# Kernel tuning notes

Measured on AMD Instinct MI355X. Metric: run time of the kernel, lower is better.

The kernel has to match this reference:

```python
import jax, jax.numpy as jnp
import numpy as np

SCALE = 2
K_UP = 5
K_ENC = 3


def _conv(x, w, b, pad):
    # NCHW conv, OIHW weights
    y = jax.lax.conv_general_dilated(
        x, w, window_strides=(1, 1), padding=((pad, pad), (pad, pad)),
        dimension_numbers=('NCHW', 'OIHW', 'NCHW'))
    return y + b[None, :, None, None]


def setup_inputs() -> dict:
    key = jax.random.key(0)
    k0, k1, k2 = jax.random.split(key, 3)
    b, c, h, w = 4, 256, 64, 64
    c_mid = 64
    n_kernel = SCALE * SCALE * K_UP * K_UP  # 100
    x = jax.random.normal(k0, (b, c, h, w), jnp.float32)
    w1 = jax.random.normal(k1, (c_mid, c, K_ENC, K_ENC), jnp.float32) * 0.02
    b1 = jnp.zeros((c_mid,), jnp.float32)
    w2 = jax.random.normal(k2, (n_kernel, c_mid, 1, 1), jnp.float32) * 0.02
    b2 = jnp.zeros((n_kernel,), jnp.float32)
    return {"x": x, "w1": w1, "b1": b1, "w2": w2, "b2": b2}


def reference(x, w1, b1, w2, b2):
    b, c, h, w = x.shape
    s, k = SCALE, K_UP
    # kernel prediction encoder: 3x3 conv -> ReLU -> 1x1 conv
    feat = jax.nn.relu(_conv(x, w1, b1, K_ENC // 2))
    kern = _conv(feat, w2, b2, 0)                     # (b, s^2*k^2, h, w)
    kern = jax.nn.softmax(kern, axis=1)               # softmax over full channel dim (as in source)
    kern = kern.reshape(b, s * s, k * k, h, w)
    # F.unfold(x, k, padding=k//2) -> (b, c, k^2, h, w); torch ordering: kh major, kw minor
    pad = k // 2
    xp = jnp.pad(x, ((0, 0), (0, 0), (pad, pad), (pad, pad)))
    patches = jnp.stack([xp[:, :, i:i + h, j:j + w]
                         for i in range(k) for j in range(k)], axis=2)  # (b, c, k^2, h, w)
    # per-pixel weighted reassembly: sum over k^2 neighborhood
    out = jnp.einsum('bskhw,bckhw->bschw', kern, patches)  # (b, s^2, c, h, w)
    # view(b, s^2*c, h, w) then pixel_shuffle(scale), exactly matching torch semantics
    out = out.reshape(b, s * s * c, h, w)
    cout = (s * s * c) // (s * s)
    out = out.reshape(b, cout, s, s, h, w)
    out = out.transpose(0, 1, 4, 2, 5, 3).reshape(b, cout, h * s, w * s)
    return out
```

## Files before the change

kernel.cpp:

```cpp
#include <hip/hip_runtime.h>


#define BB 4
#define CC 256
#define HH 64
#define WW 64
#define CMID 64
#define NKCH 100

typedef __bf16 bf16;
typedef __bf16 bf16x8 __attribute__((ext_vector_type(8)));
typedef float f32x4 __attribute__((ext_vector_type(4)));

__device__ __forceinline__ void async_copy16(const void* gsrc, void* ldst) {
    __builtin_amdgcn_global_load_lds(
        (__attribute__((address_space(1))) void*)(void*)gsrc,
        (__attribute__((address_space(3))) void*)ldst, 16, 0, 0);
}

__global__ void k0a_transform(const float* __restrict__ w1, bf16* __restrict__ w1c) {
    int c8 = blockIdx.x;
    int oq = blockIdx.y;
    int tid = threadIdx.x;
    __shared__ __align__(16) float wf[16 * 300];

    for (int i = tid; i < 16 * 72; i += 256) {
        int o = i / 72, r = i % 72;
        *(float4*)&wf[o * 300 + r * 4] =
            *(const float4*)&w1[(size_t)(oq * 16 + o) * 2304 + c8 * 288 + r * 4];
    }
    __syncthreads();

    for (int t = tid; t < 576; t += 256) {
        int o = t & 15, q = (t >> 4) & 3, kk = t >> 6;
        union { bf16 h[8]; uint4 u; } v;
        #pragma unroll
        for (int i8 = 0; i8 < 8; ++i8)
            v.h[i8] = (bf16)wf[o * 300 + (q * 8 + i8) * 9 + kk];
        *(uint4*)&w1c[(size_t)((((c8 * 9 + kk) * 4 + q) * 64) + oq * 16 + o) * 8] = v.u;
    }
}

__global__ __launch_bounds__(512) void k12_fused(const float* __restrict__ x,
        const bf16* __restrict__ w1c, const float* __restrict__ b1,
        const float* __restrict__ w2, const float* __restrict__ b2,
        float* __restrict__ kern) {
    int bh = blockIdx.x;
    int b = bh >> 6, h = bh & 63;
    int tid = threadIdx.x;
    int lane = tid & 63, wid = tid >> 6;
    int l15 = lane & 15, quad = lane >> 4;
    int mhalf = wid & 1, nq = wid >> 1;

    __shared__ __align__(16) char smem[99072];
    bf16*  xs   = (bf16*)smem;
    bf16*  wlds = (bf16*)(smem + 15872);
    float* kts  = (float*)(smem + 15872);
    float* fs   = (float*)(smem + 52736);
    float* ws2  = (float*)(smem + 69376);
    float* red  = (float*)(smem + 94976);

    for (int i = tid; i < 1600; i += 512)
        *(float4*)&ws2[i * 4] = *(const float4*)&w2[i * 4];

    for (int i = tid; i < 3 * 66 * 40; i += 512) xs[i] = (bf16)0.f;

    const float* xb = x + (size_t)b * (CC * HH * WW);

    int ppp[6], rrr[6];
    bool vmask[6];
    #pragma unroll
    for (int j = 0; j < 6; ++j) {
        int task = wid + j * 8;
        ppp[j] = task & 15;
        rrr[j] = task >> 4;
        int hr = h - 1 + rrr[j];
        vmask[j] = (hr >= 0 && hr < HH);
    }

    float f0[6], f1[6];
    #define LOADX(C8)                                                            \
        _Pragma("unroll")                                                        \
        for (int j = 0; j < 6; ++j) {                                            \
            if (vmask[j]) {                                                      \
                const float* src = xb + ((size_t)((C8) * 32 + 2 * ppp[j]) * (HH * WW)) \
                                 + (h - 1 + rrr[j]) * WW + lane;                 \
                f0[j] = src[0]; f1[j] = src[HH * WW];                            \
            }                                                                    \
        }

    LOADX(0)
    __syncthreads();

    f32x4 acc0 = {0.f, 0.f, 0.f, 0.f}, acc1 = {0.f, 0.f, 0.f, 0.f};

    for (int c8 = 0; c8 < 8; ++c8) {
        for (int t = wid; t < 36; t += 8)
            async_copy16(w1c + (((c8 * 36 + t) << 9) + lane * 8), (void*)&wlds[t << 9]);
        #pragma unroll
        for (int j = 0; j < 6; ++j) {
            if (vmask[j]) {
                union { bf16 hh[2]; unsigned u; } cv;
                cv.hh[0] = (bf16)f0[j]; cv.hh[1] = (bf16)f1[j];
                *(unsigned*)&xs[(rrr[j] * 66 + 1 + lane) * 40 + 2 * ppp[j]] = cv.u;
            }
        }
        __syncthreads();
        if (c8 < 7) { LOADX(c8 + 1) }
        #pragma unroll
        for (int kk = 0; kk < 9; ++kk) {
            int r3 = kk / 3, kw = kk % 3;
            bf16x8 a0 = *(const bf16x8*)&wlds[((kk * 4 + quad) * 64 + mhalf * 32 + l15) * 8];
            bf16x8 a1 = *(const bf16x8*)&wlds[((kk * 4 + quad) * 64 + mhalf * 32 + 16 + l15) * 8];
            bf16x8 xv = *(const bf16x8*)&xs[(r3 * 66 + nq * 16 + l15 + kw) * 40 + quad * 8];
            acc0 = __builtin_amdgcn_mfma_f32_16x16x32_bf16(a0, xv, acc0, 0, 0, 0);
            acc1 = __builtin_amdgcn_mfma_f32_16x16x32_bf16(a1, xv, acc1, 0, 0, 0);
        }
        __syncthreads();
    }

    int px = nq * 16 + l15;
    #pragma unroll
    for (int mi = 0; mi < 2; ++mi) {
        int oc0 = mhalf * 32 + mi * 16 + quad * 4;
        float4 bv = *(const float4*)&b1[oc0];
        f32x4 v = mi ? acc1 : acc0;
        fs[(oc0 + 0) * 65 + px] = fmaxf(v[0] + bv.x, 0.f);
        fs[(oc0 + 1) * 65 + px] = fmaxf(v[1] + bv.y, 0.f);
        fs[(oc0 + 2) * 65 + px] = fmaxf(v[2] + bv.z, 0.f);
        fs[(oc0 + 3) * 65 + px] = fmaxf(v[3] + bv.w, 0.f);
    }
    __syncthreads();

    int w = lane;
    int g = wid, s2 = g & 3, ihalf = g >> 2;
    int i0 = ihalf ? 13 : 0;

    float4 fv[16];
    #pragma unroll
    for (int q = 0; q < 16; ++q) {
        fv[q].x = fs[(4 * q + 0) * 65 + w];
        fv[q].y = fs[(4 * q + 1) * 65 + w];
        fv[q].z = fs[(4 * q + 2) * 65 + w];
        fv[q].w = fs[(4 * q + 3) * 65 + w];
    }

    float lg[13];
    #pragma unroll
    for (int ii = 0; ii < 13; ++ii) {
        int idx = i0 + ii;
        bool act = (idx < 25);
        int oc = s2 * 25 + (act ? idx : 0);
        float a = b2[oc];
        const float4* wr = (const float4*)&ws2[oc * 64];
        #pragma unroll
        for (int q = 0; q < 16; ++q) {
            float4 wv = wr[q];
            a += fv[q].x * wv.x + fv[q].y * wv.y + fv[q].z * wv.z + fv[q].w * wv.w;
        }
        lg[ii] = act ? a : -1e30f;
    }

    float m = -1e30f;
    #pragma unroll
    for (int ii = 0; ii < 13; ++ii) m = fmaxf(m, lg[ii]);
    red[g * 64 + w] = m;
    __syncthreads();
    m = fmaxf(fmaxf(fmaxf(red[0 * 64 + w], red[1 * 64 + w]),
                    fmaxf(red[2 * 64 + w], red[3 * 64 + w])),
              fmaxf(fmaxf(red[4 * 64 + w], red[5 * 64 + w]),
                    fmaxf(red[6 * 64 + w], red[7 * 64 + w])));
    float ssum = 0.f;
    #pragma unroll
    for (int ii = 0; ii < 13; ++ii) { lg[ii] = __expf(lg[ii] - m); ssum += lg[ii]; }
    red[512 + g * 64 + w] = ssum;
    __syncthreads();
    ssum = ((red[512 + 0 * 64 + w] + red[512 + 1 * 64 + w]) +
            (red[512 + 2 * 64 + w] + red[512 + 3 * 64 + w])) +
           ((red[512 + 4 * 64 + w] + red[512 + 5 * 64 + w]) +
            (red[512 + 6 * 64 + w] + red[512 + 7 * 64 + w]));
    float inv = 1.f / ssum;
    #pragma unroll
    for (int ii = 0; ii < 13; ++ii)
        if (i0 + ii < 25) kts[((i0 + ii) * 64 + w) * 4 + s2] = lg[ii] * inv;
    __syncthreads();

    float* kout = kern + (size_t)bh * 6400;
    for (int i = tid; i < 1600; i += 512)
        *(float4*)&kout[i * 4] = *(const float4*)&kts[i * 4];
    #undef LOADX
}

__global__ __launch_bounds__(256, 5) void k3_reassemble(const float* __restrict__ x,
        const float* __restrict__ kern, float* __restrict__ out) {
    int chunk = blockIdx.x;
    int bh = blockIdx.y;
    int b = bh >> 6, h = bh & 63;
    int tid = threadIdx.x;
    int w = tid & 63;
    int cg = tid >> 6;

    __shared__ __align__(16) float xs[5 * 68 * 20];

    for (int i = tid; i < 16 * 5 * 64; i += 256) {
        int ww = i & 63;
        int rr = (i >> 6) % 5;
        int cc = i / 320;
        int hr = h - 2 + rr;
        float v = (hr >= 0 && hr < HH)
            ? x[(((size_t)b * CC + chunk * 16 + cc) * HH + hr) * WW + ww] : 0.f;
        xs[(rr * 68 + 2 + ww) * 20 + cc] = v;
    }
    for (int i = tid; i < 320; i += 256) {
        int cc = i & 15;
        int q = (i >> 4) & 3;
        int rr = i >> 6;
        int slot = (q < 2) ? q : (q + 64);
        xs[(rr * 68 + slot) * 20 + cc] = 0.f;
    }

    const float* kp = kern + (size_t)bh * 6400 + w * 4;

    f32x4 kv0[5];
    #pragma unroll
    for (int kw = 0; kw < 5; ++kw)
        kv0[kw] = *(const f32x4*)&kp[kw * 256];

    __syncthreads();

    f32x4 a0 = {0.f,0.f,0.f,0.f}, a1 = {0.f,0.f,0.f,0.f};
    f32x4 a2 = {0.f,0.f,0.f,0.f}, a3 = {0.f,0.f,0.f,0.f};
    int cg4 = cg * 4;
    #pragma unroll
    for (int r = 0; r < 5; ++r) {
        #pragma unroll
        for (int kw = 0; kw < 5; ++kw) {
            f32x4 kv = (r == 0) ? kv0[kw]
                                : *(const f32x4*)&kp[(r * 5 + kw) * 256];
            f32x4 xv = *(const f32x4*)&xs[(r * 68 + w + kw) * 20 + cg4];
            a0 += kv.x * xv;
            a1 += kv.y * xv;
            a2 += kv.z * xv;
            a3 += kv.w * xv;
        }
    }

    int cq = chunk * 4 + cg;
    f32x4 accs[4] = {a0, a1, a2, a3};
    #pragma unroll
    for (int s = 0; s < 4; ++s) {
        size_t base = (((size_t)b * 256 + s * 64 + cq) * 128 + 2 * h) * 128 + 2 * w;
        *(float2*)&out[base]       = make_float2(accs[s][0], accs[s][1]);
        *(float2*)&out[base + 128] = make_float2(accs[s][2], accs[s][3]);
    }
}

extern "C" void kernel_launch(void* const* d_in, const int* in_sizes, int n_in,
                              void* d_out, int out_size, void* d_ws, size_t ws_size,
                              hipStream_t stream) {
    const float* x  = (const float*)d_in[0];
    const float* w1 = (const float*)d_in[1];
    const float* b1 = (const float*)d_in[2];
    const float* w2 = (const float*)d_in[3];
    const float* b2 = (const float*)d_in[4];
    float* out = (float*)d_out;

    char* wsb = (char*)d_ws;
    float* kern = (float*)wsb;
    bf16*  w1c  = (bf16*)(wsb + 6553600);

    k0a_transform<<<dim3(8, 4), 256, 0, stream>>>(w1, w1c);
    k12_fused<<<dim3(BB * HH), 512, 0, stream>>>(x, w1c, b1, w2, b2, kern);
    k3_reassemble<<<dim3(16, BB * HH), 256, 0, stream>>>(x, kern, out);
}
```

Measured before the change: 142.0 us.

## Double-buffer conv tiles, drop w2 LDS staging, swizzle reassembly LDS layout

The fused conv kernel now keeps two LDS buffers for both the x tile and the weight tile. The async weight copy and global x loads for the next channel chunk run while the MFMAs work on the current chunk, and each chunk pair needs fewer barriers. The w2 LDS staging is removed and the 1x1 conv reads w2 straight from global memory, which frees LDS for the second buffers. The reassembly kernel loads x as float4, stores it in a per-channel-group layout with an XOR swizzle to cut bank conflicts, and raises its occupancy hint from 5 to 6 blocks per CU. The larger LDS footprint may lower occupancy of the fused kernel.

```diff
diff --git a/kernel.cpp b/kernel.cpp
--- a/kernel.cpp
+++ b/kernel.cpp
@@ -52,18 +52,14 @@
     int l15 = lane & 15, quad = lane >> 4;
     int mhalf = wid & 1, nq = wid >> 1;
 
-    __shared__ __align__(16) char smem[99072];
-    bf16*  xs   = (bf16*)smem;
-    bf16*  wlds = (bf16*)(smem + 15872);
-    float* kts  = (float*)(smem + 15872);
-    float* fs   = (float*)(smem + 52736);
-    float* ws2  = (float*)(smem + 69376);
-    float* red  = (float*)(smem + 94976);
-
-    for (int i = tid; i < 1600; i += 512)
-        *(float4*)&ws2[i * 4] = *(const float4*)&w2[i * 4];
-
-    for (int i = tid; i < 3 * 66 * 40; i += 512) xs[i] = (bf16)0.f;
+    __shared__ __align__(16) char smem[122112];
+    bf16*  xs0  = (bf16*)smem;
+    bf16*  xs1  = (bf16*)(smem + 15872);
+    bf16*  wl0  = (bf16*)(smem + 31744);
+    bf16*  wl1  = (bf16*)(smem + 68608);
+    float* fs   = (float*)(smem + 105472);
+    float* kts  = (float*)(smem + 31744);
+    float* red  = (float*)smem;
 
     const float* xb = x + (size_t)b * (CC * HH * WW);
 
@@ -78,44 +74,59 @@
         vmask[j] = (hr >= 0 && hr < HH);
     }
 
-    float f0[6], f1[6];
-    #define LOADX(C8)                                                            \
+    float fA0[6], fA1[6], fB0[6], fB1[6];
+    #define LOADX(C8, F0, F1)                                                    \
         _Pragma("unroll")                                                        \
         for (int j = 0; j < 6; ++j) {                                            \
             if (vmask[j]) {                                                      \
                 const float* src = xb + ((size_t)((C8) * 32 + 2 * ppp[j]) * (HH * WW)) \
                                  + (h - 1 + rrr[j]) * WW + lane;                 \
-                f0[j] = src[0]; f1[j] = src[HH * WW];                            \
+                F0[j] = src[0]; F1[j] = src[HH * WW];                            \
             }                                                                    \
         }
-
-    LOADX(0)
+    #define WRITEB(F0, F1, XSDST)                                                \
+        _Pragma("unroll")                                                        \
+        for (int j = 0; j < 6; ++j) {                                            \
+            if (vmask[j]) {                                                      \
+                union { bf16 hh[2]; unsigned u; } cv;                            \
+                cv.hh[0] = (bf16)F0[j]; cv.hh[1] = (bf16)F1[j];                  \
+                *(unsigned*)&XSDST[(rrr[j] * 66 + 1 + lane) * 40 + 2 * ppp[j]] = cv.u; \
+            }                                                                    \
+        }
+    #define ACOPY(C8, WDST)                                                      \
+        for (int t = wid; t < 36; t += 8)                                        \
+            async_copy16(w1c + ((((C8) * 36 + t) << 9) + lane * 8), (void*)&WDST[t << 9]);
+    #define MFMAS(XSRC, WSRC)                                                    \
+        _Pragma("unroll")                                                        \
+        for (int kk = 0; kk < 9; ++kk) {                                         \
+            int r3 = kk / 3, kw = kk % 3;                                        \
+            bf16x8 a0 = *(const bf16x8*)&WSRC[((kk * 4 + quad) * 64 + mhalf * 32 + l15) * 8]; \
+            bf16x8 a1 = *(const bf16x8*)&WSRC[((kk * 4 + quad) * 64 + mhalf * 32 + 16 + l15) * 8]; \
+            bf16x8 xv = *(const bf16x8*)&XSRC[(r3 * 66 + nq * 16 + l15 + kw) * 40 + quad * 8]; \
+            acc0 = __builtin_amdgcn_mfma_f32_16x16x32_bf16(a0, xv, acc0, 0, 0, 0); \
+            acc1 = __builtin_amdgcn_mfma_f32_16x16x32_bf16(a1, xv, acc1, 0, 0, 0); \
+        }
+
+    for (int i = tid; i < 7936; i += 512) { xs0[i] = (bf16)0.f; xs1[i] = (bf16)0.f; }
+    LOADX(0, fA0, fA1)
+    ACOPY(0, wl0)
+    __syncthreads();
+    WRITEB(fA0, fA1, xs0)
+    LOADX(1, fB0, fB1)
     __syncthreads();
 
     f32x4 acc0 = {0.f, 0.f, 0.f, 0.f}, acc1 = {0.f, 0.f, 0.f, 0.f};
 
-    for (int c8 = 0; c8 < 8; ++c8) {
-        for (int t = wid; t < 36; t += 8)
-            async_copy16(w1c + (((c8 * 36 + t) << 9) + lane * 8), (void*)&wlds[t << 9]);
-        #pragma unroll
-        for (int j = 0; j < 6; ++j) {
-            if (vmask[j]) {
-                union { bf16 hh[2]; unsigned u; } cv;
-                cv.hh[0] = (bf16)f0[j]; cv.hh[1] = (bf16)f1[j];
-                *(unsigned*)&xs[(rrr[j] * 66 + 1 + lane) * 40 + 2 * ppp[j]] = cv.u;
-            }
-        }
+    for (int c8 = 0; c8 < 8; c8 += 2) {
+        ACOPY(c8 + 1, wl1)
+        MFMAS(xs0, wl0)
+        WRITEB(fB0, fB1, xs1)
+        if (c8 < 6) { LOADX(c8 + 2, fA0, fA1) }
         __syncthreads();
-        if (c8 < 7) { LOADX(c8 + 1) }
-        #pragma unroll
-        for (int kk = 0; kk < 9; ++kk) {
-            int r3 = kk / 3, kw = kk % 3;
-            bf16x8 a0 = *(const bf16x8*)&wlds[((kk * 4 + quad) * 64 + mhalf * 32 + l15) * 8];
-            bf16x8 a1 = *(const bf16x8*)&wlds[((kk * 4 + quad) * 64 + mhalf * 32 + 16 + l15) * 8];
-            bf16x8 xv = *(const bf16x8*)&xs[(r3 * 66 + nq * 16 + l15 + kw) * 40 + quad * 8];
-            acc0 = __builtin_amdgcn_mfma_f32_16x16x32_bf16(a0, xv, acc0, 0, 0, 0);
-            acc1 = __builtin_amdgcn_mfma_f32_16x16x32_bf16(a1, xv, acc1, 0, 0, 0);
-        }
+        if (c8 < 6) { ACOPY(c8 + 2, wl0) }
+        MFMAS(xs1, wl1)
+        if (c8 < 6) { WRITEB(fA0, fA1, xs0) }
+        if (c8 < 6) { LOADX(c8 + 3, fB0, fB1) }
         __syncthreads();
     }
 
@@ -152,7 +163,7 @@
         bool act = (idx < 25);
         int oc = s2 * 25 + (act ? idx : 0);
         float a = b2[oc];
-        const float4* wr = (const float4*)&ws2[oc * 64];
+        const float4* wr = (const float4*)&w2[oc * 64];
         #pragma unroll
         for (int q = 0; q < 16; ++q) {
             float4 wv = wr[q];
@@ -189,9 +200,12 @@
     for (int i = tid; i < 1600; i += 512)
         *(float4*)&kout[i * 4] = *(const float4*)&kts[i * 4];
     #undef LOADX
-}
-
-__global__ __launch_bounds__(256, 5) void k3_reassemble(const float* __restrict__ x,
+    #undef WRITEB
+    #undef ACOPY
+    #undef MFMAS
+}
+
+__global__ __launch_bounds__(256, 6) void k3_reassemble(const float* __restrict__ x,
         const float* __restrict__ kern, float* __restrict__ out) {
     int chunk = blockIdx.x;
     int bh = blockIdx.y;
@@ -200,44 +214,57 @@
     int w = tid & 63;
     int cg = tid >> 6;
 
-    __shared__ __align__(16) float xs[5 * 68 * 20];
-
-    for (int i = tid; i < 16 * 5 * 64; i += 256) {
-        int ww = i & 63;
-        int rr = (i >> 6) % 5;
-        int cc = i / 320;
+    __shared__ __align__(16) float xs[5 * 4 * 68 * 4];
+
+    #pragma unroll
+    for (int k = 0; k < 5; ++k) {
+        int idx = tid + k * 256;
+        int u = idx & 15, cc = (idx >> 4) & 15, rr = idx >> 8;
         int hr = h - 2 + rr;
-        float v = (hr >= 0 && hr < HH)
-            ? x[(((size_t)b * CC + chunk * 16 + cc) * HH + hr) * WW + ww] : 0.f;
-        xs[(rr * 68 + 2 + ww) * 20 + cc] = v;
+        float4 v = make_float4(0.f, 0.f, 0.f, 0.f);
+        if (hr >= 0 && hr < HH)
+            v = *(const float4*)&x[(((size_t)b * CC + chunk * 16 + cc) * HH + hr) * WW + 4 * u];
+        int base = (rr * 4 + (cc >> 2)) * 68;
+        int c = cc & 3;
+        #pragma unroll
+        for (int j = 0; j < 4; ++j) {
+            int s = 2 + 4 * u + j;
+            int sw = s ^ ((s >> 3) & 7);
+            xs[(base + sw) * 4 + c] = ((const float*)&v)[j];
+        }
     }
     for (int i = tid; i < 320; i += 256) {
-        int cc = i & 15;
-        int q = (i >> 4) & 3;
-        int rr = i >> 6;
+        int c = i & 3;
+        int q = (i >> 2) & 3;
+        int rg = i >> 4;
         int slot = (q < 2) ? q : (q + 64);
-        xs[(rr * 68 + slot) * 20 + cc] = 0.f;
+        xs[(rg * 68 + slot) * 4 + c] = 0.f;
     }
 
     const float* kp = kern + (size_t)bh * 6400 + w * 4;
-
     f32x4 kv0[5];
     #pragma unroll
     for (int kw = 0; kw < 5; ++kw)
         kv0[kw] = *(const f32x4*)&kp[kw * 256];
 
+    int swk[5];
+    #pragma unroll
+    for (int kw = 0; kw < 5; ++kw) {
+        int s = w + kw;
+        swk[kw] = s ^ ((s >> 3) & 7);
+    }
+
     __syncthreads();
 
     f32x4 a0 = {0.f,0.f,0.f,0.f}, a1 = {0.f,0.f,0.f,0.f};
     f32x4 a2 = {0.f,0.f,0.f,0.f}, a3 = {0.f,0.f,0.f,0.f};
-    int cg4 = cg * 4;
     #pragma unroll
     for (int r = 0; r < 5; ++r) {
         #pragma unroll
         for (int kw = 0; kw < 5; ++kw) {
             f32x4 kv = (r == 0) ? kv0[kw]
                                 : *(const f32x4*)&kp[(r * 5 + kw) * 256];
-            f32x4 xv = *(const f32x4*)&xs[(r * 68 + w + kw) * 20 + cg4];
+            f32x4 xv = *(const f32x4*)&xs[((r * 4 + cg) * 68 + swk[kw]) * 4];
             a0 += kv.x * xv;
             a1 += kv.y * xv;
             a2 += kv.z * xv;
```

Measured after the change: 132.6 us. -6.6%, faster.
